# Kernel optimization log

Measured on AMD Instinct MI355X. Metric: run time of the kernel, lower is better.

Reference implementation:

```python
import jax, jax.numpy as jnp
import numpy as np

N = 512       # num_nodes (feature dim of x == num_nodes, per GCNConv(num_nodes, f1))
BZ = 32       # subjects
TC = 256      # tc_length
F1 = 256
F2 = 128
E = 524288    # edges in the given (corr) graph over all bz*N nodes
NTOT = BZ * N
SLOPE = 0.2   # leaky relu negative_slope


def setup_inputs() -> dict:
    key = jax.random.key(0)
    ks = jax.random.split(key, 17)
    w = lambda k, shape: (jax.random.normal(k, shape, jnp.float32) * (shape[-1] ** -0.5))
    return {
        "x": jax.random.normal(ks[0], (NTOT, N), jnp.float32),
        "t": jax.random.normal(ks[1], (NTOT, TC), jnp.float32),
        "gumbel_u": jax.random.uniform(ks[2], (BZ, N, N, 2), jnp.float32),
        "edge_index": jax.random.randint(ks[3], (2, E), 0, NTOT, jnp.int64 if jax.config.jax_enable_x64 else jnp.int32),
        "conv1_w": w(ks[4], (F1, N)),
        "conv1_b": jnp.zeros((F1,), jnp.float32),
        "conv2_w": w(ks[5], (F2, F1)),
        "conv2_b": jnp.zeros((F2,), jnp.float32),
        "fc_cat_w": w(ks[6], (2, 2 * TC)),
        "fc_cat_b": jnp.zeros((2,), jnp.float32),
        "fcn1_w": w(ks[7], (256, F2 * 2 * N)),
        "fcn1_b": jnp.zeros((256,), jnp.float32),
        "fcn2_w": w(ks[8], (32, 256)),
        "fcn2_b": jnp.zeros((32,), jnp.float32),
        "fcn3_w": w(ks[9], (2, 32)),
        "fcn3_b": jnp.zeros((2,), jnp.float32),
    }


def _gcn_dense(x, A, W, b):
    # PyG GCNConv on a dense 0/1 adjacency A (edge r->c means A[r,c]=1):
    # add self loop, in-degree symmetric norm, aggregate sources into targets.
    n = A.shape[0]
    Ah = A + jnp.eye(n, dtype=A.dtype)
    deg = Ah.sum(axis=0)                                  # in-degree (targets = cols)
    dis = jnp.where(deg > 0, jax.lax.rsqrt(deg), 0.0)
    M = dis[:, None] * Ah * dis[None, :]                  # M[j,i] = d_j^-1/2 A_hat[j,i] d_i^-1/2
    return M.T @ (x @ W.T) + b


def _gcn_sparse(x, row, col, W, b):
    n = x.shape[0]
    loops = jnp.arange(n, dtype=row.dtype)
    r = jnp.concatenate([row, loops])
    c = jnp.concatenate([col, loops])
    deg = jax.ops.segment_sum(jnp.ones_like(c, x.dtype), c, num_segments=n)
    dis = jnp.where(deg > 0, jax.lax.rsqrt(deg), 0.0)
    norm = dis[r] * dis[c]                                # [E+n]
    xw = x @ W.T                                          # [n, out]
    out = jax.ops.segment_sum(xw[r] * norm[:, None], c, num_segments=n)
    return out + b


def reference(x, t, gumbel_u, edge_index, conv1_w, conv1_b, conv2_w, conv2_b,
              fc_cat_w, fc_cat_b, fcn1_w, fcn1_b, fcn2_w, fcn2_b, fcn3_w, fcn3_b):
    bz = t.shape[0] // N
    tb = t.reshape(bz, N, -1)
    xb = x.reshape(bz, N, -1)
    # fc_cat(relu(cat([senders, receivers]))) factors into per-node terms:
    Ws = fc_cat_w[:, :TC]   # multiplies senders half
    Wr = fc_cat_w[:, TC:]   # multiplies receivers half

    def per_sample(ti, xi, ui):
        u = jax.nn.relu(ti)                               # [N, TC]
        ls = u @ Ws.T                                     # [N, 2] sender term
        lr = u @ Wr.T                                     # [N, 2] receiver term
        # pair k = i*N+j has receiver t_i, sender t_j
        logits = lr[:, None, :] + ls[None, :, :] + fc_cat_b   # [N, N, 2]
        g = -jnp.log(-jnp.log(jnp.clip(ui, 1e-9, 1.0 - 1e-9)))  # Gumbel(0,1)
        y = logits + g                                    # tau = 1
        A = (jnp.argmax(y, axis=-1) == 0).astype(xi.dtype)    # hard sample, class 0 => edge
        A = jax.lax.stop_gradient(A)                      # torch.where -> indices blocks grad
        h = jax.nn.relu(_gcn_dense(xi, A, conv1_w, conv1_b))
        return _gcn_dense(h, A, conv2_w, conv2_b)         # [N, F2]

    x_op = jax.vmap(per_sample)(tb, xb, gumbel_u)         # [bz, N, F2]

    row, col = edge_index[0], edge_index[1]
    x_corr = jax.nn.relu(_gcn_sparse(x, row, col, conv1_w, conv1_b))
    x_corr = _gcn_sparse(x_corr, row, col, conv2_w, conv2_b)   # [bz*N, F2]

    emb = jnp.concatenate([x_op.reshape(-1, F2), x_corr], axis=1)  # [bz*N, 2*F2]
    emb = emb.reshape(bz, -1)                             # [bz, 2*F2*N]
    h = jax.nn.leaky_relu(emb @ fcn1_w.T + fcn1_b, SLOPE)
    h = jax.nn.leaky_relu(h @ fcn2_w.T + fcn2_b, SLOPE)
    return h @ fcn3_w.T + fcn3_b                          # [bz, 2]
```

## Files before the change

### kernel.cpp

```cpp
#include <hip/hip_runtime.h>
#include <hip/hip_bf16.h>

typedef __bf16 bf16_t;
typedef __bf16 bf16x8 __attribute__((ext_vector_type(8)));
typedef __bf16 bf16x4 __attribute__((ext_vector_type(4)));
typedef float f32x4 __attribute__((ext_vector_type(4)));

constexpr int kN = 512;
constexpr int kBZ = 32;
constexpr int kTC = 256;
constexpr int kE = 524288;
constexpr int kNTOT = 16384;

__device__ __forceinline__ void gll16(const bf16_t* g, bf16_t* l) {
    __builtin_amdgcn_global_load_lds((const __attribute__((address_space(1))) void*)g,
                                     (__attribute__((address_space(3))) void*)l, 16, 0, 0);
}

__device__ __forceinline__ void stage128x64(const bf16_t* __restrict__ src, int ld,
                                            bf16_t* lds, int wave, int lane) {
#pragma unroll
    for (int i = 0; i < 4; i++) {
        int r0 = (wave * 4 + i) * 8;
        int r = r0 + (lane >> 3);
        int c = (lane & 7) ^ (r & 7);
        gll16(src + (size_t)r * ld + c * 8, lds + r0 * 64);
    }
}

__device__ __forceinline__ bf16x8 rdfrag(const bf16_t* lds, int row, int cc) {
    return *(const bf16x8*)(lds + row * 64 + ((cc ^ (row & 7)) * 8));
}

__global__ __launch_bounds__(256) void k_front(const float* __restrict__ c1w, const float* __restrict__ c2w,
                                               bf16_t* __restrict__ c1b, bf16_t* __restrict__ c2b,
                                               int* __restrict__ counts, float* __restrict__ degsum,
                                               const float* __restrict__ tin, const float* __restrict__ fcw,
                                               const float* __restrict__ fcb, float4* __restrict__ lsr) {
    int b = blockIdx.x;
    if (b < 192) {
        int i = b * 256 + threadIdx.x;
        const int n0 = 32768, n1 = n0 + 8192, n2 = n1 + 4096, n3 = n2 + 4096;
        if (i < n0) {
            float4 v = ((const float4*)c1w)[i];
            bf16x4 o = {(bf16_t)v.x, (bf16_t)v.y, (bf16_t)v.z, (bf16_t)v.w};
            ((bf16x4*)c1b)[i] = o;
        } else if (i < n1) {
            int j = i - n0;
            float4 v = ((const float4*)c2w)[j];
            bf16x4 o = {(bf16_t)v.x, (bf16_t)v.y, (bf16_t)v.z, (bf16_t)v.w};
            ((bf16x4*)c2b)[j] = o;
        } else if (i < n2) {
            ((int4*)counts)[i - n1] = make_int4(0, 0, 0, 0);
        } else if (i < n3) {
            ((float4*)degsum)[i - n2] = make_float4(0.f, 0.f, 0.f, 0.f);
        }
    } else {
        int row = (b - 192) * 4 + (threadIdx.x >> 6);
        int lane = threadIdx.x & 63;
        const float* tr = tin + (size_t)row * kTC;
        float s0 = 0, s1 = 0, r0 = 0, r1 = 0;
        for (int k = lane; k < kTC; k += 64) {
            float u = fmaxf(tr[k], 0.f);
            s0 += u * fcw[k];
            s1 += u * fcw[512 + k];
            r0 += u * fcw[256 + k];
            r1 += u * fcw[768 + k];
        }
#pragma unroll
        for (int off = 32; off > 0; off >>= 1) {
            s0 += __shfl_down(s0, off); s1 += __shfl_down(s1, off);
            r0 += __shfl_down(r0, off); r1 += __shfl_down(r1, off);
        }
        if (lane == 0) lsr[row] = make_float4(s0 + fcb[0], s1 + fcb[1], r0, r1);
    }
}

__global__ __launch_bounds__(256) void k_adjhist(const float* __restrict__ gum, const float4* __restrict__ lsr,
                                                 bf16_t* __restrict__ AT, float* __restrict__ degsum,
                                                 const int* __restrict__ col, int* __restrict__ counts) {
    int blk = blockIdx.x;
    if (blk >= 2048) {
        int e = (blk - 2048) * 256 + threadIdx.x;
        if (e < kE) atomicAdd(&counts[col[e]], 1);
        return;
    }
    int s = blk >> 6;
    int a0 = ((blk >> 3) & 7) * 64, b0 = (blk & 7) * 64;
    __shared__ bf16_t tile[64][72];
    int t = threadIdx.x;
    int lb = t & 63, ra = t >> 6;
    int b = b0 + lb;
    float4 pb = lsr[s * kN + b];
#pragma unroll 4
    for (int p = 0; p < 16; p++) {
        int a = a0 + p * 4 + ra;
        float4 qa = lsr[s * kN + a];
        float2 gv = *(const float2*)(gum + ((((size_t)s * kN + a) * kN + b) << 1));
        float u0 = fmaxf(gv.x, 1e-9f);
        float u1 = fmaxf(gv.y, 1e-9f);
        float g0 = -__logf(-__logf(u0));
        float g1 = -__logf(-__logf(u1));
        float v = ((qa.z + pb.x + g0) >= (qa.w + pb.y + g1)) ? 1.f : 0.f;
        if (a == b) v += 1.f;
        tile[lb][p * 4 + ra] = (bf16_t)v;
    }
    __syncthreads();
    int rj = t >> 3, li = (t & 7) * 8;
#pragma unroll
    for (int p = 0; p < 2; p++) {
        int j = p * 32 + rj;
        bf16x8 v = *(const bf16x8*)&tile[j][li];
        *(bf16x8*)(AT + ((size_t)s * kN + b0 + j) * kN + a0 + li) = v;
        float ps = 0;
#pragma unroll
        for (int q = 0; q < 8; q++) ps += (float)v[q];
        ps += __shfl_down(ps, 4);
        ps += __shfl_down(ps, 2);
        ps += __shfl_down(ps, 1);
        if ((t & 7) == 0) atomicAdd(degsum + s * kN + b0 + j, ps);
    }
}

template <int MODE, int GDEC>
__global__ __launch_bounds__(256) void k_gemm(const bf16_t* __restrict__ A, const bf16_t* __restrict__ B,
                                              bf16_t* __restrict__ C, int K, int lda, int ldb, int ldc,
                                              size_t sA, size_t sB, size_t sC,
                                              const float* __restrict__ degsum, const float* __restrict__ bias) {
    int m0, n0, s;
    {
        int f = blockIdx.x;
        if constexpr (GDEC == 1) {
            int p = ((f >> 4) << 3) | (f & 7);
            int y = (f >> 3) & 1;
            s = p >> 2;
            m0 = (p & 3) * 128;
            n0 = y * 128;
        } else {
            s = ((f >> 5) << 3) | (f & 7);
            m0 = ((f >> 3) & 3) * 128;
            n0 = 0;
        }
    }
    const bf16_t* Ab = A + sA * s + (size_t)m0 * lda;
    const bf16_t* Bb = B + sB * s + (size_t)n0 * ldb;
    C += sC * s;
    __shared__ __align__(16) bf16_t As[2][128 * 64], Bs[2][128 * 64];
    f32x4 acc[4][4] = {};
    int tid = threadIdx.x;
    int wave = tid >> 6, lane = tid & 63;
    int wm = (wave & 1) * 64, wn = (wave >> 1) * 64;
    int fm = lane & 15, fq = lane >> 4;
    stage128x64(Ab, lda, As[0], wave, lane);
    stage128x64(Bb, ldb, Bs[0], wave, lane);
    int cur = 0;
    for (int kb = 0;;) {
        int kn = kb + 64;
        __syncthreads();
        if (kn < K) {
            stage128x64(Ab + kn, lda, As[cur ^ 1], wave, lane);
            stage128x64(Bb + kn, ldb, Bs[cur ^ 1], wave, lane);
        }
#pragma unroll
        for (int kk = 0; kk < 2; kk++) {
            bf16x8 af[4], bfr[4];
#pragma unroll
            for (int i = 0; i < 4; i++) {
                af[i] = rdfrag(As[cur], wm + i * 16 + fm, kk * 4 + fq);
                bfr[i] = rdfrag(Bs[cur], wn + i * 16 + fm, kk * 4 + fq);
            }
#pragma unroll
            for (int i = 0; i < 4; i++)
#pragma unroll
                for (int j = 0; j < 4; j++)
                    acc[i][j] = __builtin_amdgcn_mfma_f32_16x16x32_bf16(af[i], bfr[j], acc[i][j], 0, 0, 0);
        }
        kb = kn;
        if (kb >= K) break;
        cur ^= 1;
    }
#pragma unroll
    for (int i = 0; i < 4; i++) {
#pragma unroll
        for (int r = 0; r < 4; r++) {
            int row = wm + i * 16 + fq * 4 + r;
            float sc = rsqrtf(degsum[(size_t)s * kN + m0 + row]);
#pragma unroll
            for (int j = 0; j < 4; j++) {
                int col = n0 + wn + j * 16 + fm;
                float v = sc * acc[i][j][r] + bias[col];
                if constexpr (MODE == 1) v = fmaxf(v, 0.f);
                C[(size_t)(m0 + row) * ldc + col] = (bf16_t)v;
            }
        }
    }
}

template <bool AF32, int F, int DENSE_ROWS, bool PAIRXY>
__global__ __launch_bounds__(256) void k_gemmT(const void* __restrict__ Ap, const bf16_t* __restrict__ B,
                                               bf16_t* __restrict__ XW, bf16_t* __restrict__ ZT, int K,
                                               const float* __restrict__ degsum) {
    int m0, n0;
    if constexpr (PAIRXY) {
        int f = blockIdx.x;
        m0 = (((f >> 4) << 3) | (f & 7)) * 128;
        n0 = ((f >> 3) & 1) * 128;
    } else {
        m0 = blockIdx.x * 128;
        n0 = blockIdx.y * 128;
    }
    constexpr int AST = AF32 ? 9216 : 8192;
    __shared__ __align__(16) bf16_t smem[2 * AST + 2 * 8192];
    bf16_t* A0 = smem;
    bf16_t* A1 = smem + AST;
    bf16_t* B0 = smem + 2 * AST;
    bf16_t* B1 = smem + 2 * AST + 8192;
    f32x4 acc[4][4] = {};
    int tid = threadIdx.x;
    int wave = tid >> 6, lane = tid & 63;
    int wm = (wave & 1) * 64, wn = (wave >> 1) * 64;
    int fm = lane & 15, fq = lane >> 4;
    int srow = tid >> 3, scol = (tid & 7) * 8;
    const float* Af = (const float*)Ap;
    const bf16_t* Abf = (const bf16_t*)Ap;
    if constexpr (AF32) {
#pragma unroll
        for (int p = 0; p < 4; p++) {
            int row = p * 32 + srow;
            const float* ap = Af + (size_t)(m0 + row) * K + scol;
            float4 lo = *(const float4*)ap, hi = *(const float4*)(ap + 4);
            bf16x8 o = {(bf16_t)lo.x, (bf16_t)lo.y, (bf16_t)lo.z, (bf16_t)lo.w,
                        (bf16_t)hi.x, (bf16_t)hi.y, (bf16_t)hi.z, (bf16_t)hi.w};
            *(bf16x8*)&A0[row * 72 + scol] = o;
        }
    } else {
        stage128x64(Abf + (size_t)m0 * K, K, A0, wave, lane);
    }
    stage128x64(B + (size_t)n0 * K, K, B0, wave, lane);
    int cur = 0;
    for (int kb = 0;;) {
        int kn = kb + 64;
        bool more = kn < K;
        bf16_t* Ac = cur ? A1 : A0;
        bf16_t* An = cur ? A0 : A1;
        bf16_t* Bc = cur ? B1 : B0;
        bf16_t* Bn = cur ? B0 : B1;
        float4 plo[4], phi[4];
        __syncthreads();
        if (more) {
            if constexpr (AF32) {
#pragma unroll
                for (int p = 0; p < 4; p++) {
                    int row = p * 32 + srow;
                    const float* ap = Af + (size_t)(m0 + row) * K + kn + scol;
                    plo[p] = *(const float4*)ap;
                    phi[p] = *(const float4*)(ap + 4);
                }
            } else {
                stage128x64(Abf + (size_t)m0 * K + kn, K, An, wave, lane);
            }
            stage128x64(B + (size_t)n0 * K + kn, K, Bn, wave, lane);
        }
#pragma unroll
        for (int kk = 0; kk < 2; kk++) {
            bf16x8 af[4], bfr[4];
#pragma unroll
            for (int i = 0; i < 4; i++) {
                if constexpr (AF32)
                    af[i] = *(const bf16x8*)&Ac[(wm + i * 16 + fm) * 72 + kk * 32 + fq * 8];
                else
                    af[i] = rdfrag(Ac, wm + i * 16 + fm, kk * 4 + fq);
                bfr[i] = rdfrag(Bc, wn + i * 16 + fm, kk * 4 + fq);
            }
#pragma unroll
            for (int i = 0; i < 4; i++)
#pragma unroll
                for (int j = 0; j < 4; j++)
                    acc[i][j] = __builtin_amdgcn_mfma_f32_16x16x32_bf16(af[i], bfr[j], acc[i][j], 0, 0, 0);
        }
        if constexpr (AF32) {
            if (more) {
#pragma unroll
                for (int p = 0; p < 4; p++) {
                    int row = p * 32 + srow;
                    bf16x8 o = {(bf16_t)plo[p].x, (bf16_t)plo[p].y, (bf16_t)plo[p].z, (bf16_t)plo[p].w,
                                (bf16_t)phi[p].x, (bf16_t)phi[p].y, (bf16_t)phi[p].z, (bf16_t)phi[p].w};
                    *(bf16x8*)&An[row * 72 + scol] = o;
                }
            }
        }
        kb = kn;
        if (kb >= K) break;
        cur ^= 1;
    }
    bool doT = (m0 < DENSE_ROWS);
    __syncthreads();
#pragma unroll
    for (int i = 0; i < 4; i++) {
#pragma unroll
        for (int r = 0; r < 4; r++) {
            int row = wm + i * 16 + fq * 4 + r;
            float sc = doT ? rsqrtf(degsum[m0 + row]) : 0.f;
#pragma unroll
            for (int j = 0; j < 4; j++) {
                int col = wn + j * 16 + fm;
                float v = acc[i][j][r];
                XW[(size_t)(m0 + row) * F + n0 + col] = (bf16_t)v;
                if (doT) smem[col * 136 + row] = (bf16_t)(sc * v);
            }
        }
    }
    if (doT) {
        __syncthreads();
        int fr = tid >> 1, hi = (tid & 1) * 64;
        bf16_t* zrow = ZT + ((size_t)(m0 >> 9) * F + n0 + fr) * kN + (m0 & 511) + hi;
#pragma unroll
        for (int q = 0; q < 8; q++)
            *(bf16x8*)(zrow + q * 8) = *(const bf16x8*)&smem[fr * 136 + hi + q * 8];
    }
}


__global__ __launch_bounds__(1024) void k_scan(const int* __restrict__ counts, int* __restrict__ offsets,
                                               int* __restrict__ cursor, float* __restrict__ dis_s) {
    __shared__ int ldc_[16896];
    __shared__ int sums[1024];
    int t = threadIdx.x;
#define IDX(j) ((j) + ((j) >> 5))
    for (int i = 0; i < 16; i++) {
        int g = i * 1024 + t;
        int c = counts[g];
        ldc_[IDX(g)] = c;
        dis_s[g] = rsqrtf((float)(c + 1));
    }
    __syncthreads();
    int s = 0;
    for (int i = 0; i < 16; i++) s += ldc_[IDX(t * 16 + i)];
    sums[t] = s;
    __syncthreads();
    for (int off = 1; off < 1024; off <<= 1) {
        int y = (t >= off) ? sums[t - off] : 0;
        __syncthreads();
        sums[t] += y;
        __syncthreads();
    }
    int run = sums[t] - s;
    for (int i = 0; i < 16; i++) {
        int j = t * 16 + i;
        int c = ldc_[IDX(j)];
        ldc_[IDX(j)] = run;
        run += c;
    }
    __syncthreads();
    for (int i = 0; i < 16; i++) {
        int g = i * 1024 + t;
        int o = ldc_[IDX(g)];
        offsets[g] = o;
        cursor[g] = o;
    }
#undef IDX
}

__global__ __launch_bounds__(256) void k_fill(const int* __restrict__ row, const int* __restrict__ col,
                                              int* __restrict__ cursor, int* __restrict__ list) {
    int e = blockIdx.x * 256 + threadIdx.x;
    if (e < kE) {
        int p = atomicAdd(&cursor[col[e]], 1);
        list[p] = row[e];
    }
}

template <int F, bool RELU>
__global__ __launch_bounds__(256) void k_sagg(const bf16_t* __restrict__ XW, int rowOffIn,
                                              const int* __restrict__ list, const int* __restrict__ offsets,
                                              const int* __restrict__ counts, const float* __restrict__ dis_s,
                                              const float* __restrict__ bias, bf16_t* __restrict__ OUT,
                                              int outColOff) {
    constexpr int TPR = F / 8;
    constexpr int RPB = 256 / TPR;
    int j = blockIdx.x * RPB + threadIdx.x / TPR;
    int f8 = (threadIdx.x % TPR) * 8;
    float dj = dis_s[j];
    const bf16_t* base = XW + (size_t)rowOffIn * F;
    float acc[8];
    {
        bf16x8 v = *(const bf16x8*)(base + (size_t)j * F + f8);
#pragma unroll
        for (int q = 0; q < 8; q++) acc[q] = dj * (float)v[q];
    }
    int off = offsets[j], cnt = counts[j];
    int e = 0;
    int nb = cnt & ~7;
    if (nb) {
        int r[8];
#pragma unroll
        for (int q = 0; q < 8; q++) r[q] = list[off + q];
        while (true) {
            int en = e + 8;
            bool more = en < nb;
            int rn[8];
            if (more) {
#pragma unroll
                for (int q = 0; q < 8; q++) rn[q] = list[off + en + q];
            }
            float d[8];
#pragma unroll
            for (int q = 0; q < 8; q++) d[q] = dis_s[r[q]];
            bf16x8 v0 = *(const bf16x8*)(base + (size_t)r[0] * F + f8);
            bf16x8 v1 = *(const bf16x8*)(base + (size_t)r[1] * F + f8);
            bf16x8 v2 = *(const bf16x8*)(base + (size_t)r[2] * F + f8);
            bf16x8 v3 = *(const bf16x8*)(base + (size_t)r[3] * F + f8);
            bf16x8 v4 = *(const bf16x8*)(base + (size_t)r[4] * F + f8);
            bf16x8 v5 = *(const bf16x8*)(base + (size_t)r[5] * F + f8);
            bf16x8 v6 = *(const bf16x8*)(base + (size_t)r[6] * F + f8);
            bf16x8 v7 = *(const bf16x8*)(base + (size_t)r[7] * F + f8);
#pragma unroll
            for (int q = 0; q < 8; q++)
                acc[q] += ((d[0] * (float)v0[q] + d[1] * (float)v1[q]) + (d[2] * (float)v2[q] + d[3] * (float)v3[q])) +
                          ((d[4] * (float)v4[q] + d[5] * (float)v5[q]) + (d[6] * (float)v6[q] + d[7] * (float)v7[q]));
            e = en;
            if (!more) break;
#pragma unroll
            for (int q = 0; q < 8; q++) r[q] = rn[q];
        }
    }
    for (; e + 4 <= cnt; e += 4) {
        int r0 = list[off + e], r1 = list[off + e + 1], r2 = list[off + e + 2], r3 = list[off + e + 3];
        float d0 = dis_s[r0], d1 = dis_s[r1], d2 = dis_s[r2], d3 = dis_s[r3];
        bf16x8 v0 = *(const bf16x8*)(base + (size_t)r0 * F + f8);
        bf16x8 v1 = *(const bf16x8*)(base + (size_t)r1 * F + f8);
        bf16x8 v2 = *(const bf16x8*)(base + (size_t)r2 * F + f8);
        bf16x8 v3 = *(const bf16x8*)(base + (size_t)r3 * F + f8);
#pragma unroll
        for (int q = 0; q < 8; q++)
            acc[q] += (d0 * (float)v0[q] + d1 * (float)v1[q]) + (d2 * (float)v2[q] + d3 * (float)v3[q]);
    }
    for (; e < cnt; e++) {
        int r = list[off + e];
        float d = dis_s[r];
        bf16x8 v = *(const bf16x8*)(base + (size_t)r * F + f8);
#pragma unroll
        for (int q = 0; q < 8; q++) acc[q] += d * (float)v[q];
    }
    bf16x8 o;
#pragma unroll
    for (int q = 0; q < 8; q++) {
        float v = dj * acc[q] + bias[f8 + q];
        if (RELU) v = fmaxf(v, 0.f);
        o[q] = (bf16_t)v;
    }
    *(bf16x8*)(OUT + (size_t)j * 256 + outColOff + f8) = o;
}

__global__ __launch_bounds__(256) void k_fcn1(const bf16_t* __restrict__ EMB, const float* __restrict__ W1,
                                              float* __restrict__ partials) {
    int tid = threadIdx.x, wave = tid >> 6, lane = tid & 63;
    int fm = lane & 15, fq = lane >> 4;
    int kb0 = blockIdx.x * 512;
    f32x4 acc[2][4] = {};
#pragma unroll 4
    for (int ks = 0; ks < 512; ks += 32) {
        int k = kb0 + ks + fq * 8;
        bf16x8 a0 = *(const bf16x8*)(EMB + (size_t)fm * 131072 + k);
        bf16x8 a1 = *(const bf16x8*)(EMB + (size_t)(16 + fm) * 131072 + k);
        bf16x8 bfr[4];
#pragma unroll
        for (int j = 0; j < 4; j++) {
            int n = wave * 64 + j * 16 + fm;
            const float* p = W1 + (size_t)n * 131072 + k;
            float4 lo = *(const float4*)p;
            float4 hi = *(const float4*)(p + 4);
            bf16x8 b = {(bf16_t)lo.x, (bf16_t)lo.y, (bf16_t)lo.z, (bf16_t)lo.w,
                        (bf16_t)hi.x, (bf16_t)hi.y, (bf16_t)hi.z, (bf16_t)hi.w};
            bfr[j] = b;
        }
#pragma unroll
        for (int j = 0; j < 4; j++) {
            acc[0][j] = __builtin_amdgcn_mfma_f32_16x16x32_bf16(a0, bfr[j], acc[0][j], 0, 0, 0);
            acc[1][j] = __builtin_amdgcn_mfma_f32_16x16x32_bf16(a1, bfr[j], acc[1][j], 0, 0, 0);
        }
    }
    float* P = partials + (size_t)blockIdx.x * 8192;
#pragma unroll
    for (int i = 0; i < 2; i++)
#pragma unroll
        for (int j = 0; j < 4; j++)
#pragma unroll
            for (int r = 0; r < 4; r++)
                P[(size_t)(i * 16 + fq * 4 + r) * 256 + wave * 64 + j * 16 + fm] = acc[i][j][r];
}

__global__ __launch_bounds__(256) void k_reduce(const float* __restrict__ partials, float* __restrict__ h1pre) {
    __shared__ float red[8][32];
    int t = threadIdx.x;
    int el = t & 31, q = t >> 5;
    int e = blockIdx.x * 32 + el;
    float s = 0;
#pragma unroll 8
    for (int i = 0; i < 32; i++) s += partials[(size_t)(q * 32 + i) * 8192 + e];
    red[q][el] = s;
    __syncthreads();
    if (t < 32) {
        float r = 0;
#pragma unroll
        for (int qq = 0; qq < 8; qq++) r += red[qq][t];
        h1pre[blockIdx.x * 32 + t] = r;
    }
}

__global__ __launch_bounds__(256) void k_head(const float* __restrict__ h1pre, const float* __restrict__ b1,
                                              const float* __restrict__ W2, const float* __restrict__ b2,
                                              const float* __restrict__ W3, const float* __restrict__ b3,
                                              float* __restrict__ out) {
    __shared__ float h1s[32][256];
    __shared__ float h2s[32][32];
    int t = threadIdx.x;
    for (int i = 0; i < 32; i++) {
        float s = h1pre[i * 256 + t] + b1[t];
        h1s[i][t] = (s > 0.f) ? s : 0.2f * s;
    }
    __syncthreads();
    for (int p = 0; p < 4; p++) {
        int id = p * 256 + t, si = id >> 5, o2 = id & 31;
        float s = 0;
        for (int k = 0; k < 256; k++) s += h1s[si][k] * W2[o2 * 256 + k];
        s += b2[o2];
        h2s[si][o2] = (s > 0.f) ? s : 0.2f * s;
    }
    __syncthreads();
    if (t < 64) {
        int si = t >> 1, o3 = t & 1;
        float s = 0;
#pragma unroll
        for (int k = 0; k < 32; k++) s += h2s[si][k] * W3[o3 * 32 + k];
        out[si * 2 + o3] = s + b3[o3];
    }
}


extern "C" void kernel_launch(void* const* d_in, const int* in_sizes, int n_in,
                              void* d_out, int out_size, void* d_ws, size_t ws_size,
                              hipStream_t stream) {
    const float* x = (const float*)d_in[0];
    const float* t = (const float*)d_in[1];
    const float* gum = (const float*)d_in[2];
    const int* eidx = (const int*)d_in[3];
    const float* c1w = (const float*)d_in[4];
    const float* c1b = (const float*)d_in[5];
    const float* c2w = (const float*)d_in[6];
    const float* c2b = (const float*)d_in[7];
    const float* fcw = (const float*)d_in[8];
    const float* fcb = (const float*)d_in[9];
    const float* w1 = (const float*)d_in[10];
    const float* b1 = (const float*)d_in[11];
    const float* w2 = (const float*)d_in[12];
    const float* b2 = (const float*)d_in[13];
    const float* w3 = (const float*)d_in[14];
    const float* b3 = (const float*)d_in[15];
    float* out = (float*)d_out;
    (void)in_sizes; (void)n_in; (void)out_size; (void)ws_size;

    char* ws = (char*)d_ws;
    size_t off = 0;
    auto alloc = [&](size_t bytes) -> char* {
        char* p = ws + off;
        off += (bytes + 255) & ~size_t(255);
        return p;
    };
    bf16_t* c1wb = (bf16_t*)alloc((size_t)256 * 512 * 2);
    bf16_t* c2wb = (bf16_t*)alloc((size_t)128 * 256 * 2);
    float4* lsr = (float4*)alloc((size_t)kNTOT * 16);
    bf16_t* AT = (bf16_t*)alloc((size_t)kBZ * kN * kN * 2);
    float* degsum = (float*)alloc((size_t)kNTOT * 4);
    bf16_t* XW1_EMB = (bf16_t*)alloc((size_t)kNTOT * 256 * 2);
    bf16_t* Z1T = (bf16_t*)alloc((size_t)kBZ * 256 * 512 * 2);
    bf16_t* H = (bf16_t*)alloc((size_t)32768 * 256 * 2);
    bf16_t* XW2 = (bf16_t*)alloc((size_t)32768 * 128 * 2);
    bf16_t* Z2T = (bf16_t*)alloc((size_t)kBZ * 128 * 512 * 2);
    int* counts = (int*)alloc((size_t)kNTOT * 4);
    int* offsets = (int*)alloc((size_t)kNTOT * 4);
    int* cursor = (int*)alloc((size_t)kNTOT * 4);
    float* diss = (float*)alloc((size_t)kNTOT * 4);
    int* list = (int*)alloc((size_t)kE * 4);
    float* partials = (float*)alloc((size_t)256 * 8192 * 4);
    float* h1pre = (float*)alloc((size_t)8192 * 4);

    bf16_t* XW1 = XW1_EMB;
    bf16_t* EMB = XW1_EMB;

    k_front<<<4288, 256, 0, stream>>>(c1w, c2w, c1wb, c2wb, counts, degsum, t, fcw, fcb, lsr);
    k_adjhist<<<4096, 256, 0, stream>>>(gum, lsr, AT, degsum, eidx + kE, counts);
    k_scan<<<1, 1024, 0, stream>>>(counts, offsets, cursor, diss);
    k_fill<<<2048, 256, 0, stream>>>(eidx, eidx + kE, cursor, list);
    k_gemmT<true, 256, kNTOT, true><<<256, 256, 0, stream>>>(x, c1wb, XW1, Z1T, 512, degsum);
    k_gemm<1, 1><<<256, 256, 0, stream>>>(AT, Z1T, H, 512, 512, 512, 256,
                                          (size_t)512 * 512, (size_t)256 * 512, (size_t)512 * 256,
                                          degsum, c1b);
    k_sagg<256, true><<<2048, 256, 0, stream>>>(XW1, 0, list, offsets, counts, diss, c1b,
                                                H + (size_t)16384 * 256, 0);
    k_gemmT<false, 128, kNTOT, false><<<dim3(256, 1, 1), 256, 0, stream>>>(H, c2wb, XW2, Z2T, 256, degsum);
    k_gemm<2, 2><<<128, 256, 0, stream>>>(AT, Z2T, EMB, 512, 512, 512, 256,
                                          (size_t)512 * 512, (size_t)128 * 512, (size_t)512 * 256,
                                          degsum, c2b);
    k_sagg<128, false><<<1024, 256, 0, stream>>>(XW2, 16384, list, offsets, counts, diss, c2b, EMB, 128);
    k_fcn1<<<256, 256, 0, stream>>>(EMB, w1, partials);
    k_reduce<<<256, 256, 0, stream>>>(partials, h1pre);
    k_head<<<1, 256, 0, stream>>>(h1pre, b1, w2, b2, w3, b3, out);
}
```

Before: 484.7 us.

## Fuse dense GCN layer-1 aggregation with layer-2 weight GEMM per subject tile

Adds a kernel that, for each 64-row tile of a subject's dense adjacency, computes the first GCN aggregation with bias and ReLU, keeps the hidden tile in LDS, and multiplies it straight away by the second conv weight to write the normalized Z2T. This avoids writing the dense-path H to global memory and reading it back in a separate transform GEMM. The remaining transform GEMM now covers only the sparse-path half with half the grid. The cost is a larger LDS footprint per block and narrower 64-row tiles, which may lower occupancy and data reuse.

Measured after the change: 482.4 us. About the same (-0.5%).

```diff
diff --git a/kernel.cpp b/kernel.cpp
--- a/kernel.cpp
+++ b/kernel.cpp
@@ -17,11 +17,12 @@
                                      (__attribute__((address_space(3))) void*)l, 16, 0, 0);
 }
 
-__device__ __forceinline__ void stage128x64(const bf16_t* __restrict__ src, int ld,
-                                            bf16_t* lds, int wave, int lane) {
-#pragma unroll
-    for (int i = 0; i < 4; i++) {
-        int r0 = (wave * 4 + i) * 8;
+template <int NI>
+__device__ __forceinline__ void stageT(const bf16_t* __restrict__ src, int ld,
+                                       bf16_t* lds, int wave, int lane) {
+#pragma unroll
+    for (int i = 0; i < NI; i++) {
+        int r0 = (wave * NI + i) * 8;
         int r = r0 + (lane >> 3);
         int c = (lane & 7) ^ (r & 7);
         gll16(src + (size_t)r * ld + c * 8, lds + r0 * 64);
@@ -130,17 +131,9 @@
     int m0, n0, s;
     {
         int f = blockIdx.x;
-        if constexpr (GDEC == 1) {
-            int p = ((f >> 4) << 3) | (f & 7);
-            int y = (f >> 3) & 1;
-            s = p >> 2;
-            m0 = (p & 3) * 128;
-            n0 = y * 128;
-        } else {
-            s = ((f >> 5) << 3) | (f & 7);
-            m0 = ((f >> 3) & 3) * 128;
-            n0 = 0;
-        }
+        s = ((f >> 5) << 3) | (f & 7);
+        m0 = ((f >> 3) & 3) * 128;
+        n0 = 0;
     }
     const bf16_t* Ab = A + sA * s + (size_t)m0 * lda;
     const bf16_t* Bb = B + sB * s + (size_t)n0 * ldb;
@@ -151,15 +144,15 @@
     int wave = tid >> 6, lane = tid & 63;
     int wm = (wave & 1) * 64, wn = (wave >> 1) * 64;
     int fm = lane & 15, fq = lane >> 4;
-    stage128x64(Ab, lda, As[0], wave, lane);
-    stage128x64(Bb, ldb, Bs[0], wave, lane);
+    stageT<4>(Ab, lda, As[0], wave, lane);
+    stageT<4>(Bb, ldb, Bs[0], wave, lane);
     int cur = 0;
     for (int kb = 0;;) {
         int kn = kb + 64;
         __syncthreads();
         if (kn < K) {
-            stage128x64(Ab + kn, lda, As[cur ^ 1], wave, lane);
-            stage128x64(Bb + kn, ldb, Bs[cur ^ 1], wave, lane);
+            stageT<4>(Ab + kn, lda, As[cur ^ 1], wave, lane);
+            stageT<4>(Bb + kn, ldb, Bs[cur ^ 1], wave, lane);
         }
 #pragma unroll
         for (int kk = 0; kk < 2; kk++) {
@@ -193,6 +186,131 @@
                 C[(size_t)(m0 + row) * ldc + col] = (bf16_t)v;
             }
         }
+    }
+}
+
+__global__ __launch_bounds__(256) void k_gcn1f(const bf16_t* __restrict__ AT, const bf16_t* __restrict__ Z1T,
+                                               const bf16_t* __restrict__ C2W, const float* __restrict__ degsum,
+                                               const float* __restrict__ c1b, bf16_t* __restrict__ Z2T) {
+    int f = blockIdx.x;
+    int s = ((f >> 6) << 3) | (f & 7);
+    int mt = (f >> 3) & 7;
+    const bf16_t* Ab = AT + (size_t)s * (512 * 512) + (size_t)(mt * 64) * 512;
+    const bf16_t* Bb = Z1T + (size_t)s * (256 * 512);
+    __shared__ __align__(16) bf16_t smem[40960];
+    bf16_t* Hs = smem;
+    int tid = threadIdx.x, wave = tid >> 6, lane = tid & 63;
+    int fm = lane & 15, fq = lane >> 4;
+    f32x4 acc[4][4] = {};
+    stageT<2>(Ab, 512, smem, wave, lane);
+    stageT<8>(Bb, 512, smem + 8192, wave, lane);
+    int cur = 0;
+    for (int kb = 0;;) {
+        int kn = kb + 64;
+        bf16_t* Ac = cur ? smem + 4096 : smem;
+        bf16_t* An = cur ? smem : smem + 4096;
+        bf16_t* Bc = cur ? smem + 24576 : smem + 8192;
+        bf16_t* Bn = cur ? smem + 8192 : smem + 24576;
+        __syncthreads();
+        if (kn < 512) {
+            stageT<2>(Ab + kn, 512, An, wave, lane);
+            stageT<8>(Bb + kn, 512, Bn, wave, lane);
+        }
+        int wn = wave * 64;
+#pragma unroll
+        for (int kk = 0; kk < 2; kk++) {
+            bf16x8 af[4], bfr[4];
+#pragma unroll
+            for (int i = 0; i < 4; i++) {
+                af[i] = rdfrag(Ac, i * 16 + fm, kk * 4 + fq);
+                bfr[i] = rdfrag(Bc, wn + i * 16 + fm, kk * 4 + fq);
+            }
+#pragma unroll
+            for (int i = 0; i < 4; i++)
+#pragma unroll
+                for (int j = 0; j < 4; j++)
+                    acc[i][j] = __builtin_amdgcn_mfma_f32_16x16x32_bf16(af[i], bfr[j], acc[i][j], 0, 0, 0);
+        }
+        kb = kn;
+        if (kb >= 512) break;
+        cur ^= 1;
+    }
+    __syncthreads();
+    stageT<4>(C2W, 256, smem + 16384, wave, lane);
+    {
+        int wn = wave * 64;
+#pragma unroll
+        for (int i = 0; i < 4; i++) {
+#pragma unroll
+            for (int r = 0; r < 4; r++) {
+                int row = i * 16 + fq * 4 + r;
+                float sc = rsqrtf(degsum[(size_t)s * 512 + mt * 64 + row]);
+#pragma unroll
+                for (int j = 0; j < 4; j++) {
+                    int col = wn + j * 16 + fm;
+                    float v = fmaxf(sc * acc[i][j][r] + c1b[col], 0.f);
+                    int c = col >> 3;
+                    int cS = (c & 24) | ((c & 7) ^ (row & 7));
+                    Hs[row * 256 + cS * 8 + (col & 7)] = (bf16_t)v;
+                }
+            }
+        }
+    }
+    f32x4 acc2[4][2] = {};
+    int cur2 = 0;
+    for (int kb2 = 0;;) {
+        int kn2 = kb2 + 64;
+        bf16_t* B2c = cur2 ? smem + 24576 : smem + 16384;
+        bf16_t* B2n = cur2 ? smem + 16384 : smem + 24576;
+        __syncthreads();
+        if (kn2 < 256) stageT<4>(C2W + kn2, 256, B2n, wave, lane);
+        int wc = wave * 32;
+#pragma unroll
+        for (int kk = 0; kk < 2; kk++) {
+            int cbase = (kb2 >> 3) + kk * 4 + fq;
+            bf16x8 af2[4], bfr2[2];
+#pragma unroll
+            for (int i = 0; i < 4; i++) {
+                int row = i * 16 + fm;
+                int cS = (cbase & 24) | ((cbase & 7) ^ (row & 7));
+                af2[i] = *(const bf16x8*)&Hs[row * 256 + cS * 8];
+            }
+#pragma unroll
+            for (int j = 0; j < 2; j++) bfr2[j] = rdfrag(B2c, wc + j * 16 + fm, kk * 4 + fq);
+#pragma unroll
+            for (int i = 0; i < 4; i++)
+#pragma unroll
+                for (int j = 0; j < 2; j++)
+                    acc2[i][j] = __builtin_amdgcn_mfma_f32_16x16x32_bf16(af2[i], bfr2[j], acc2[i][j], 0, 0, 0);
+        }
+        kb2 = kn2;
+        if (kb2 >= 256) break;
+        cur2 ^= 1;
+    }
+    __syncthreads();
+    {
+        int wc = wave * 32;
+#pragma unroll
+        for (int i = 0; i < 4; i++) {
+#pragma unroll
+            for (int r = 0; r < 4; r++) {
+                int row = i * 16 + fq * 4 + r;
+                float sc = rsqrtf(degsum[(size_t)s * 512 + mt * 64 + row]);
+#pragma unroll
+                for (int j = 0; j < 2; j++) {
+                    int fcol = wc + j * 16 + fm;
+                    smem[fcol * 72 + row] = (bf16_t)(sc * acc2[i][j][r]);
+                }
+            }
+        }
+    }
+    __syncthreads();
+    {
+        int fr = tid >> 1, half = tid & 1;
+        bf16_t* zp = Z2T + ((size_t)(s * 128 + fr)) * 512 + mt * 64 + half * 32;
+        const bf16_t* tp = &smem[fr * 72 + half * 32];
+#pragma unroll
+        for (int q = 0; q < 4; q++) *(bf16x8*)(zp + q * 8) = *(const bf16x8*)(tp + q * 8);
     }
 }
 
@@ -234,9 +352,9 @@
             *(bf16x8*)&A0[row * 72 + scol] = o;
         }
     } else {
-        stage128x64(Abf + (size_t)m0 * K, K, A0, wave, lane);
-    }
-    stage128x64(B + (size_t)n0 * K, K, B0, wave, lane);
+        stageT<4>(Abf + (size_t)m0 * K, K, A0, wave, lane);
+    }
+    stageT<4>(B + (size_t)n0 * K, K, B0, wave, lane);
     int cur = 0;
     for (int kb = 0;;) {
         int kn = kb + 64;
@@ -257,9 +375,9 @@
                     phi[p] = *(const float4*)(ap + 4);
                 }
             } else {
-                stage128x64(Abf + (size_t)m0 * K + kn, K, An, wave, lane);
-            }
-            stage128x64(B + (size_t)n0 * K + kn, K, Bn, wave, lane);
+                stageT<4>(Abf + (size_t)m0 * K + kn, K, An, wave, lane);
+            }
+            stageT<4>(B + (size_t)n0 * K + kn, K, Bn, wave, lane);
         }
 #pragma unroll
         for (int kk = 0; kk < 2; kk++) {
@@ -593,12 +711,11 @@
     k_scan<<<1, 1024, 0, stream>>>(counts, offsets, cursor, diss);
     k_fill<<<2048, 256, 0, stream>>>(eidx, eidx + kE, cursor, list);
     k_gemmT<true, 256, kNTOT, true><<<256, 256, 0, stream>>>(x, c1wb, XW1, Z1T, 512, degsum);
-    k_gemm<1, 1><<<256, 256, 0, stream>>>(AT, Z1T, H, 512, 512, 512, 256,
-                                          (size_t)512 * 512, (size_t)256 * 512, (size_t)512 * 256,
-                                          degsum, c1b);
+    k_gcn1f<<<256, 256, 0, stream>>>(AT, Z1T, c2wb, degsum, c1b, Z2T);
     k_sagg<256, true><<<2048, 256, 0, stream>>>(XW1, 0, list, offsets, counts, diss, c1b,
                                                 H + (size_t)16384 * 256, 0);
-    k_gemmT<false, 128, kNTOT, false><<<dim3(256, 1, 1), 256, 0, stream>>>(H, c2wb, XW2, Z2T, 256, degsum);
+    k_gemmT<false, 128, 0, false><<<dim3(128, 1, 1), 256, 0, stream>>>(H + (size_t)16384 * 256, c2wb,
+                                                                       XW2 + (size_t)16384 * 128, Z2T, 256, degsum);
     k_gemm<2, 2><<<128, 256, 0, stream>>>(AT, Z2T, EMB, 512, 512, 512, 256,
                                           (size_t)512 * 512, (size_t)128 * 512, (size_t)512 * 256,
                                           degsum, c2b);
```
